# Optimization experiments

Measured on AMD Instinct MI355X. Metric: run time of the kernel, lower is better.

Reference implementation:

```python
import jax, jax.numpy as jnp
import numpy as np

E = 8       # expert_number
TOP_K = 2


def setup_inputs() -> dict:
    key = jax.random.key(0)
    ks = jax.random.split(key, 5)
    B, S, D, H = 4, 2048, 1024, 4096
    scale = 0.02
    return {
        "x": jax.random.normal(ks[0], (B, S, D), dtype=jnp.float32),
        "gate_w": jax.random.normal(ks[1], (D, E), dtype=jnp.float32) * scale,
        "gate_b": jnp.zeros((E,), dtype=jnp.float32),
        "w1": jax.random.normal(ks[2], (E, D, H), dtype=jnp.float32) * scale,
        "b1": jnp.zeros((E, H), dtype=jnp.float32),
        "w2": jax.random.normal(ks[3], (E, H, D), dtype=jnp.float32) * scale,
        "b2": jnp.zeros((E, D), dtype=jnp.float32),
    }


def reference(x, gate_w, gate_b, w1, b1, w2, b2):
    B, S, D = x.shape
    h = x.reshape(-1, D)                                   # [T, D]

    # Router: softmax in fp32, top-k, renormalize (matches torch code)
    router_logits = h @ gate_w + gate_b                    # [T, E]
    probs = jax.nn.softmax(router_logits.astype(jnp.float32), axis=-1)
    rw, sel = jax.lax.top_k(probs, TOP_K)                  # [T, K] each
    rw = rw / rw.sum(axis=-1, keepdims=True)
    rw = rw.astype(h.dtype)

    # Per-token combine weight for each expert (0 if not selected): [T, E]
    we = (jax.nn.one_hot(sel, E, dtype=h.dtype) * rw[..., None]).sum(axis=1)

    out = jnp.zeros_like(h)
    for e in range(E):  # fixed small expert count; per-expert GEMM + weighted combine
        mid = jax.nn.gelu(h @ w1[e] + b1[e], approximate=False)  # [T, H]
        ye = mid @ w2[e] + b2[e]                                 # [T, D]
        out = out + we[:, e:e + 1] * ye

    return out.reshape(B, S, D), router_logits
```

## Files before the change

kernel.cpp:

```cpp
#include <hip/hip_runtime.h>
#include <hip/hip_bf16.h>
#include <math.h>

#define T_TOKENS 8192
#define DDIM 1024
#define HDIM 4096
#define NEXP 8
#define CAP 8192
#define MAXTILES 136

typedef __bf16 bf16;
typedef __bf16 bf16x2 __attribute__((ext_vector_type(2)));
typedef __bf16 bf16x4 __attribute__((ext_vector_type(4)));
typedef __bf16 bf16x8 __attribute__((ext_vector_type(8)));
typedef float  floatx4 __attribute__((ext_vector_type(4)));

__device__ static inline void async_load16(const void* g, void* l)
{
    __builtin_amdgcn_global_load_lds(
        (const __attribute__((address_space(1))) void*)g,
        (__attribute__((address_space(3))) void*)l, 16, 0, 0);
}

__global__ void router_kernel(const float* __restrict__ x,
                              const float* __restrict__ gw,
                              const float* __restrict__ gbias,
                              float* __restrict__ logits_out,
                              int* counts, int* token_of,
                              int* selpack, int* slots, float* wts)
{
    int t = blockIdx.x;
    int l = threadIdx.x;
    const float4* xr = (const float4*)(x + (size_t)t * DDIM);

    float p[NEXP];
#pragma unroll
    for (int e = 0; e < NEXP; ++e) p[e] = 0.f;

#pragma unroll
    for (int it = 0; it < 4; ++it) {
        int d4 = it * 64 + l;
        float4 v = xr[d4];
        float vv[4] = {v.x, v.y, v.z, v.w};
#pragma unroll
        for (int j = 0; j < 4; ++j) {
            const float4* g4 = (const float4*)(gw + (size_t)(d4 * 4 + j) * NEXP);
            float4 ga = g4[0], gb4 = g4[1];
            p[0] += vv[j] * ga.x;  p[1] += vv[j] * ga.y;
            p[2] += vv[j] * ga.z;  p[3] += vv[j] * ga.w;
            p[4] += vv[j] * gb4.x; p[5] += vv[j] * gb4.y;
            p[6] += vv[j] * gb4.z; p[7] += vv[j] * gb4.w;
        }
    }
#pragma unroll
    for (int e = 0; e < NEXP; ++e) {
#pragma unroll
        for (int off = 32; off; off >>= 1) p[e] += __shfl_xor(p[e], off);
        p[e] += gbias[e];
    }
    if (l < NEXP) logits_out[(size_t)t * NEXP + l] = p[l];

    if (l == 0) {
        int e0 = 0;
#pragma unroll
        for (int e = 1; e < NEXP; ++e) if (p[e] > p[e0]) e0 = e;
        int e1 = -1;
#pragma unroll
        for (int e = 0; e < NEXP; ++e) {
            if (e == e0) continue;
            if (e1 < 0 || p[e] > p[e1]) e1 = e;
        }
        float w0 = 1.f / (1.f + expf(p[e1] - p[e0]));
        float w1 = 1.f / (1.f + expf(p[e0] - p[e1]));
        int s0 = atomicAdd(&counts[e0], 1);
        int s1 = atomicAdd(&counts[e1], 1);
        token_of[e0 * CAP + s0] = t;
        token_of[e1 * CAP + s1] = t;
        selpack[t] = e0 | (e1 << 8);
        slots[2 * t]     = s0;
        slots[2 * t + 1] = s1;
        wts[2 * t]     = w0;
        wts[2 * t + 1] = w1;
    }
}

__global__ void offsets_kernel(const int* __restrict__ counts,
                               int* __restrict__ offsets,
                               int* __restrict__ tiles,
                               int* __restrict__ ntiles)
{
    if (threadIdx.x == 0) {
        int a = 0, nt = 0;
        for (int e = 0; e < NEXP; ++e) {
            offsets[e] = a;
            for (int r = 0; r < counts[e]; r += 128)
                tiles[nt++] = (e << 24) | (a + r);
            a += counts[e];
        }
        offsets[NEXP] = a;
        *ntiles = nt;
    }
}

__global__ void gather_kernel(const float* __restrict__ x,
                              const int* __restrict__ offsets,
                              const int* __restrict__ token_of,
                              bf16* __restrict__ xg)
{
    int row = blockIdx.x * 4 + (threadIdx.x >> 6);
    int l = threadIdx.x & 63;
    int e = 0;
#pragma unroll
    for (int i = 1; i < NEXP; ++i) e += (row >= offsets[i]);
    int t = token_of[e * CAP + (row - offsets[e])];
    const float4* src = (const float4*)(x + (size_t)t * DDIM);
    bf16x4* dst = (bf16x4*)(xg + (size_t)row * DDIM);
#pragma unroll
    for (int it = 0; it < 4; ++it) {
        float4 v = src[it * 64 + l];
        bf16x4 b;
        b[0] = (bf16)v.x; b[1] = (bf16)v.y; b[2] = (bf16)v.z; b[3] = (bf16)v.w;
        dst[it * 64 + l] = b;
    }
}

__global__ void transpose_cvt_kernel(const float* __restrict__ in,
                                     bf16* __restrict__ out, int R, int C)
{
    __shared__ bf16 tile[64][68];
    int e = blockIdx.z;
    const float* src = in + (size_t)e * R * C;
    bf16* dst = out + (size_t)e * R * C;
    int r0 = blockIdx.y * 64, c0 = blockIdx.x * 64;
    int t = threadIdx.x;
    int lr = t >> 4, c4 = t & 15;
#pragma unroll
    for (int it = 0; it < 4; ++it) {
        int r = lr + it * 16;
        float4 v = *(const float4*)(src + (size_t)(r0 + r) * C + c0 + c4 * 4);
        bf16x4 b;
        b[0] = (bf16)v.x; b[1] = (bf16)v.y; b[2] = (bf16)v.z; b[3] = (bf16)v.w;
        *(bf16x4*)(&tile[r][c4 * 4]) = b;
    }
    __syncthreads();
    int oc = t >> 3, rseg = (t & 7) * 8;
#pragma unroll
    for (int it = 0; it < 2; ++it) {
        int c = oc + it * 32;
        bf16x8 v;
#pragma unroll
        for (int j = 0; j < 8; ++j) v[j] = tile[rseg + j][c];
        *(bf16x8*)(dst + (size_t)(c0 + c) * R + r0 + rseg) = v;
    }
}

template<int KTOT>
__device__ static inline void stage_tile(const bf16* __restrict__ gbase,
                                         bf16* lds, int wave, int lane, int valid)
{
#pragma unroll
    for (int it = 0; it < 4; ++it) {
        int rbase = wave * 32 + it * 8;
        int rloc  = rbase + (lane >> 3);
        int grow  = rloc < valid ? rloc : (valid - 1);
        int chunk = (lane & 7) ^ (rloc & 7);
        const bf16* g = gbase + (size_t)grow * KTOT + chunk * 8;
        async_load16(g, lds + rbase * 64);
    }
}

__device__ static inline float fast_gelu(float v)
{
    float z = v * (2.302236479f + 0.1029451170f * v * v);
    float ex = __builtin_amdgcn_exp2f(z);
    return v * ex * __builtin_amdgcn_rcpf(ex + 1.f);
}

template<int KTOT, int NTOT, bool DOGELU, typename OutT>
__global__ __launch_bounds__(256, 4)
void moe_gemm(const bf16* __restrict__ Abase, const bf16* __restrict__ Bbase,
              const float* __restrict__ bias, OutT* __restrict__ Out,
              const int* __restrict__ tiles, const int* __restrict__ ntiles,
              const int* __restrict__ offsets)
{
    if (blockIdx.x >= *ntiles) return;
    int info = tiles[blockIdx.x];
    int e = info >> 24, row0 = info & 0xffffff;
    int valid = offsets[e + 1] - row0; if (valid > 128) valid = 128;
    int n0 = blockIdx.y * 128;

    const bf16* A = Abase + (size_t)row0 * KTOT;
    const bf16* B = Bbase + (size_t)e * NTOT * KTOT + (size_t)n0 * KTOT;
    const float* bvec = bias + (size_t)e * NTOT + n0;

    __shared__ __align__(16) bf16 As[128 * 64];
    __shared__ __align__(16) bf16 Bs[128 * 64];

    int tid = threadIdx.x;
    int lane = tid & 63, wave = tid >> 6;
    int wr = wave >> 1, wc = wave & 1;
    int m16 = lane & 15, quad = lane >> 4;
    int swz = m16 & 7;

    floatx4 acc[4][4];
#pragma unroll
    for (int i = 0; i < 4; ++i)
#pragma unroll
        for (int j = 0; j < 4; ++j)
#pragma unroll
            for (int r = 0; r < 4; ++r) acc[i][j][r] = 0.f;

    for (int k0 = 0; k0 < KTOT; k0 += 64) {
        stage_tile<KTOT>(A + k0, As, wave, lane, valid);
        stage_tile<KTOT>(B + k0, Bs, wave, lane, 128);
        __syncthreads();
#pragma unroll
        for (int ks = 0; ks < 64; ks += 32) {
            int cbase = (ks >> 3) + quad;
            int pchunk = (cbase ^ swz) * 8;
            bf16x8 af[4], bfr[4];
#pragma unroll
            for (int i = 0; i < 4; ++i)
                af[i] = *(const bf16x8*)(&As[(wr * 64 + i * 16 + m16) * 64 + pchunk]);
#pragma unroll
            for (int j = 0; j < 4; ++j)
                bfr[j] = *(const bf16x8*)(&Bs[(wc * 64 + j * 16 + m16) * 64 + pchunk]);
#pragma unroll
            for (int i = 0; i < 4; ++i)
#pragma unroll
                for (int j = 0; j < 4; ++j)
                    acc[i][j] = __builtin_amdgcn_mfma_f32_16x16x32_bf16(
                        af[i], bfr[j], acc[i][j], 0, 0, 0);
        }
        __syncthreads();
    }

#pragma unroll
    for (int i = 0; i < 4; ++i) {
#pragma unroll
        for (int r = 0; r < 4; ++r) {
            int lrow = wr * 64 + i * 16 + quad * 4 + r;
            if (lrow >= valid) continue;
            size_t orow = (size_t)(row0 + lrow) * NTOT + n0;
#pragma unroll
            for (int j = 0; j < 4; ++j) {
                int lcol = wc * 64 + j * 16 + m16;
                float v = acc[i][j][r] + bvec[lcol];
                if (DOGELU) v = fast_gelu(v);
                Out[orow + lcol] = (OutT)v;
            }
        }
    }
}

__global__ void combine_kernel(const float* __restrict__ y,
                               const int* __restrict__ offsets,
                               const int* __restrict__ selpack,
                               const int* __restrict__ slots,
                               const float* __restrict__ wts,
                               float* __restrict__ out)
{
    int t = blockIdx.x;
    int sp = selpack[t];
    int e0 = sp & 0xff, e1 = (sp >> 8) & 0xff;
    int p0 = offsets[e0] + slots[2 * t];
    int p1 = offsets[e1] + slots[2 * t + 1];
    float w0 = wts[2 * t], w1 = wts[2 * t + 1];
    const float4* y0 = (const float4*)(y + (size_t)p0 * DDIM);
    const float4* y1 = (const float4*)(y + (size_t)p1 * DDIM);
    float4* o = (float4*)(out + (size_t)t * DDIM);
    int tid = threadIdx.x;
    float4 a = y0[tid], b = y1[tid];
    float4 rr;
    rr.x = w0 * a.x + w1 * b.x;
    rr.y = w0 * a.y + w1 * b.y;
    rr.z = w0 * a.z + w1 * b.z;
    rr.w = w0 * a.w + w1 * b.w;
    o[tid] = rr;
}

extern "C" void kernel_launch(void* const* d_in, const int* in_sizes, int n_in,
                              void* d_out, int out_size, void* d_ws, size_t ws_size,
                              hipStream_t stream)
{
    (void)in_sizes; (void)n_in; (void)out_size; (void)ws_size;
    const float* x  = (const float*)d_in[0];
    const float* gw = (const float*)d_in[1];
    const float* gb = (const float*)d_in[2];
    const float* w1 = (const float*)d_in[3];
    const float* b1 = (const float*)d_in[4];
    const float* w2 = (const float*)d_in[5];
    const float* b2 = (const float*)d_in[6];
    float* out    = (float*)d_out;
    float* logits = out + (size_t)T_TOKENS * DDIM;

    char* ws = (char*)d_ws;
    const size_t MB = 1024 * 1024;
    int*   counts   = (int*)(ws + 0);
    int*   offsets  = (int*)(ws + 256);
    int*   tiles    = (int*)(ws + 512);
    int*   ntiles   = (int*)(ws + 512 + 1024);
    int*   selpack  = (int*)(ws + 4096);
    int*   slots    = (int*)(ws + 4096 + 32 * 1024);
    float* wts      = (float*)(ws + 4096 + 96 * 1024);
    int*   token_of = (int*)(ws + 4096 + 160 * 1024);
    bf16*  xg  = (bf16*)(ws + 1 * MB);
    bf16*  w1b = (bf16*)(ws + 33 * MB);
    bf16*  w2b = (bf16*)(ws + 97 * MB);
    bf16*  mid = (bf16*)(ws + 161 * MB);
    float* y   = (float*)(ws + 289 * MB);

    hipMemsetAsync(counts, 0, 32, stream);

    router_kernel<<<T_TOKENS, 64, 0, stream>>>(x, gw, gb, logits, counts,
                                               token_of, selpack, slots, wts);
    offsets_kernel<<<1, 64, 0, stream>>>(counts, offsets, tiles, ntiles);
    gather_kernel<<<2 * T_TOKENS / 4, 256, 0, stream>>>(x, offsets, token_of, xg);
    transpose_cvt_kernel<<<dim3(HDIM / 64, DDIM / 64, NEXP), 256, 0, stream>>>(
        w1, w1b, DDIM, HDIM);
    transpose_cvt_kernel<<<dim3(DDIM / 64, HDIM / 64, NEXP), 256, 0, stream>>>(
        w2, w2b, HDIM, DDIM);
    moe_gemm<DDIM, HDIM, true, bf16><<<dim3(MAXTILES, HDIM / 128), 256, 0, stream>>>(
        xg, w1b, b1, mid, tiles, ntiles, offsets);
    moe_gemm<HDIM, DDIM, false, float><<<dim3(MAXTILES, DDIM / 128), 256, 0, stream>>>(
        mid, w2b, b2, y, tiles, ntiles, offsets);
    combine_kernel<<<T_TOKENS, 256, 0, stream>>>(y, offsets, selpack, slots, wts, out);
}
```

Baseline: 970.5 us.

## Fuse combine into second GEMM via atomics, switch to 32x32 MFMA, interleave tiles

The combine kernel and the fp32 intermediate y buffer are removed. The second GEMM now scales each row by its routing weight and atomically adds it into the zero-initialised output. Both GEMMs switch from 16x16x32 to 32x32x16 MFMA instructions. The tile list is interleaved across experts, with -1 padding in place of a tile count, and the router now packs 4 tokens per block. Atomic float adds make the summation order nondeterministic, and the output now needs a memset.

Result: slower. 1.049 ms (+8.1%).

```diff
diff --git a/kernel.cpp b/kernel.cpp
--- a/kernel.cpp
+++ b/kernel.cpp
@@ -10,10 +10,9 @@
 #define MAXTILES 136
 
 typedef __bf16 bf16;
-typedef __bf16 bf16x2 __attribute__((ext_vector_type(2)));
 typedef __bf16 bf16x4 __attribute__((ext_vector_type(4)));
 typedef __bf16 bf16x8 __attribute__((ext_vector_type(8)));
-typedef float  floatx4 __attribute__((ext_vector_type(4)));
+typedef float  floatx16 __attribute__((ext_vector_type(16)));
 
 __device__ static inline void async_load16(const void* g, void* l)
 {
@@ -26,11 +25,11 @@
                               const float* __restrict__ gw,
                               const float* __restrict__ gbias,
                               float* __restrict__ logits_out,
-                              int* counts, int* token_of,
-                              int* selpack, int* slots, float* wts)
-{
-    int t = blockIdx.x;
-    int l = threadIdx.x;
+                              int* counts, int* token_of, float* wtab,
+                              int* selpack)
+{
+    int t = blockIdx.x * 4 + (threadIdx.x >> 6);
+    int l = threadIdx.x & 63;
     const float4* xr = (const float4*)(x + (size_t)t * DDIM);
 
     float p[NEXP];
@@ -76,29 +75,32 @@
         int s1 = atomicAdd(&counts[e1], 1);
         token_of[e0 * CAP + s0] = t;
         token_of[e1 * CAP + s1] = t;
+        wtab[e0 * CAP + s0] = w0;
+        wtab[e1 * CAP + s1] = w1;
         selpack[t] = e0 | (e1 << 8);
-        slots[2 * t]     = s0;
-        slots[2 * t + 1] = s1;
-        wts[2 * t]     = w0;
-        wts[2 * t + 1] = w1;
     }
 }
 
 __global__ void offsets_kernel(const int* __restrict__ counts,
                                int* __restrict__ offsets,
-                               int* __restrict__ tiles,
-                               int* __restrict__ ntiles)
+                               int* __restrict__ tiles)
 {
     if (threadIdx.x == 0) {
+        int tmp[MAXTILES];
         int a = 0, nt = 0;
         for (int e = 0; e < NEXP; ++e) {
             offsets[e] = a;
             for (int r = 0; r < counts[e]; r += 128)
-                tiles[nt++] = (e << 24) | (a + r);
+                tmp[nt++] = (e << 24) | (a + r);
             a += counts[e];
         }
         offsets[NEXP] = a;
-        *ntiles = nt;
+        int per = (nt + 7) >> 3;
+        for (int p = 0; p < MAXTILES; ++p) {
+            int c = p & 7, k = p >> 3;
+            int src = c * per + k;
+            tiles[p] = (k < per && src < nt) ? tmp[src] : -1;
+        }
     }
 }
 
@@ -176,107 +178,118 @@
     return v * ex * __builtin_amdgcn_rcpf(ex + 1.f);
 }
 
-template<int KTOT, int NTOT, bool DOGELU, typename OutT>
+#define GEMM_CORE(KTOT)                                                        \
+    int tid = threadIdx.x;                                                     \
+    int lane = tid & 63, wave = tid >> 6;                                      \
+    int wr = wave >> 1, wc = wave & 1;                                         \
+    int m32 = lane & 31, khalf = lane >> 5;                                    \
+    int swz = m32 & 7;                                                         \
+    floatx16 acc[2][2];                                                        \
+    _Pragma("unroll") for (int i = 0; i < 2; ++i)                              \
+    _Pragma("unroll") for (int j = 0; j < 2; ++j)                              \
+    _Pragma("unroll") for (int r = 0; r < 16; ++r) acc[i][j][r] = 0.f;         \
+    for (int k0 = 0; k0 < KTOT; k0 += 64) {                                    \
+        stage_tile<KTOT>(A + k0, As, wave, lane, valid);                       \
+        stage_tile<KTOT>(B + k0, Bs, wave, lane, 128);                         \
+        __syncthreads();                                                       \
+        _Pragma("unroll") for (int s = 0; s < 4; ++s) {                        \
+            int pofs = (((2 * s + khalf) ^ swz) * 8);                          \
+            bf16x8 af[2], bfr[2];                                              \
+            _Pragma("unroll") for (int i = 0; i < 2; ++i)                      \
+                af[i] = *(const bf16x8*)(&As[(wr * 64 + i * 32 + m32) * 64 + pofs]); \
+            _Pragma("unroll") for (int j = 0; j < 2; ++j)                      \
+                bfr[j] = *(const bf16x8*)(&Bs[(wc * 64 + j * 32 + m32) * 64 + pofs]); \
+            _Pragma("unroll") for (int i = 0; i < 2; ++i)                      \
+            _Pragma("unroll") for (int j = 0; j < 2; ++j)                      \
+                acc[i][j] = __builtin_amdgcn_mfma_f32_32x32x16_bf16(           \
+                    af[i], bfr[j], acc[i][j], 0, 0, 0);                        \
+        }                                                                      \
+        __syncthreads();                                                       \
+    }
+
 __global__ __launch_bounds__(256, 4)
-void moe_gemm(const bf16* __restrict__ Abase, const bf16* __restrict__ Bbase,
-              const float* __restrict__ bias, OutT* __restrict__ Out,
-              const int* __restrict__ tiles, const int* __restrict__ ntiles,
-              const int* __restrict__ offsets)
-{
-    if (blockIdx.x >= *ntiles) return;
+void moe_gemm1(const bf16* __restrict__ Abase, const bf16* __restrict__ Bbase,
+               const float* __restrict__ bias, bf16* __restrict__ Out,
+               const int* __restrict__ tiles, const int* __restrict__ offsets)
+{
     int info = tiles[blockIdx.x];
+    if (info < 0) return;
     int e = info >> 24, row0 = info & 0xffffff;
     int valid = offsets[e + 1] - row0; if (valid > 128) valid = 128;
     int n0 = blockIdx.y * 128;
 
-    const bf16* A = Abase + (size_t)row0 * KTOT;
-    const bf16* B = Bbase + (size_t)e * NTOT * KTOT + (size_t)n0 * KTOT;
-    const float* bvec = bias + (size_t)e * NTOT + n0;
+    const bf16* A = Abase + (size_t)row0 * DDIM;
+    const bf16* B = Bbase + (size_t)e * HDIM * DDIM + (size_t)n0 * DDIM;
+    const float* bvec = bias + (size_t)e * HDIM + n0;
 
     __shared__ __align__(16) bf16 As[128 * 64];
     __shared__ __align__(16) bf16 Bs[128 * 64];
 
-    int tid = threadIdx.x;
-    int lane = tid & 63, wave = tid >> 6;
-    int wr = wave >> 1, wc = wave & 1;
-    int m16 = lane & 15, quad = lane >> 4;
-    int swz = m16 & 7;
-
-    floatx4 acc[4][4];
-#pragma unroll
-    for (int i = 0; i < 4; ++i)
-#pragma unroll
-        for (int j = 0; j < 4; ++j)
-#pragma unroll
-            for (int r = 0; r < 4; ++r) acc[i][j][r] = 0.f;
-
-    for (int k0 = 0; k0 < KTOT; k0 += 64) {
-        stage_tile<KTOT>(A + k0, As, wave, lane, valid);
-        stage_tile<KTOT>(B + k0, Bs, wave, lane, 128);
-        __syncthreads();
-#pragma unroll
-        for (int ks = 0; ks < 64; ks += 32) {
-            int cbase = (ks >> 3) + quad;
-            int pchunk = (cbase ^ swz) * 8;
-            bf16x8 af[4], bfr[4];
-#pragma unroll
-            for (int i = 0; i < 4; ++i)
-                af[i] = *(const bf16x8*)(&As[(wr * 64 + i * 16 + m16) * 64 + pchunk]);
-#pragma unroll
-            for (int j = 0; j < 4; ++j)
-                bfr[j] = *(const bf16x8*)(&Bs[(wc * 64 + j * 16 + m16) * 64 + pchunk]);
-#pragma unroll
-            for (int i = 0; i < 4; ++i)
-#pragma unroll
-                for (int j = 0; j < 4; ++j)
-                    acc[i][j] = __builtin_amdgcn_mfma_f32_16x16x32_bf16(
-                        af[i], bfr[j], acc[i][j], 0, 0, 0);
-        }
-        __syncthreads();
-    }
-
-#pragma unroll
-    for (int i = 0; i < 4; ++i) {
-#pragma unroll
-        for (int r = 0; r < 4; ++r) {
-            int lrow = wr * 64 + i * 16 + quad * 4 + r;
-            if (lrow >= valid) continue;
-            size_t orow = (size_t)(row0 + lrow) * NTOT + n0;
-#pragma unroll
-            for (int j = 0; j < 4; ++j) {
-                int lcol = wc * 64 + j * 16 + m16;
-                float v = acc[i][j][r] + bvec[lcol];
-                if (DOGELU) v = fast_gelu(v);
-                Out[orow + lcol] = (OutT)v;
+    GEMM_CORE(DDIM)
+
+#pragma unroll
+    for (int i = 0; i < 2; ++i) {
+#pragma unroll
+        for (int j = 0; j < 2; ++j) {
+            int lcol = wc * 64 + j * 32 + m32;
+            float bj = bvec[lcol];
+#pragma unroll
+            for (int r = 0; r < 16; ++r) {
+                int lrow = wr * 64 + i * 32 + (r & 3) + 8 * (r >> 2) + 4 * khalf;
+                if (lrow >= valid) continue;
+                float v = acc[i][j][r] + bj;
+                Out[(size_t)(row0 + lrow) * HDIM + n0 + lcol] = (bf16)fast_gelu(v);
             }
         }
     }
 }
 
-__global__ void combine_kernel(const float* __restrict__ y,
-                               const int* __restrict__ offsets,
-                               const int* __restrict__ selpack,
-                               const int* __restrict__ slots,
-                               const float* __restrict__ wts,
-                               float* __restrict__ out)
-{
-    int t = blockIdx.x;
-    int sp = selpack[t];
-    int e0 = sp & 0xff, e1 = (sp >> 8) & 0xff;
-    int p0 = offsets[e0] + slots[2 * t];
-    int p1 = offsets[e1] + slots[2 * t + 1];
-    float w0 = wts[2 * t], w1 = wts[2 * t + 1];
-    const float4* y0 = (const float4*)(y + (size_t)p0 * DDIM);
-    const float4* y1 = (const float4*)(y + (size_t)p1 * DDIM);
-    float4* o = (float4*)(out + (size_t)t * DDIM);
-    int tid = threadIdx.x;
-    float4 a = y0[tid], b = y1[tid];
-    float4 rr;
-    rr.x = w0 * a.x + w1 * b.x;
-    rr.y = w0 * a.y + w1 * b.y;
-    rr.z = w0 * a.z + w1 * b.z;
-    rr.w = w0 * a.w + w1 * b.w;
-    o[tid] = rr;
+__global__ __launch_bounds__(256, 4)
+void moe_gemm2(const bf16* __restrict__ Abase, const bf16* __restrict__ Bbase,
+               const float* __restrict__ bias, float* __restrict__ out,
+               const int* __restrict__ tiles, const int* __restrict__ offsets,
+               const int* __restrict__ token_of, const float* __restrict__ wtab)
+{
+    int info = tiles[blockIdx.x];
+    if (info < 0) return;
+    int e = info >> 24, row0 = info & 0xffffff;
+    int valid = offsets[e + 1] - row0; if (valid > 128) valid = 128;
+    int n0 = blockIdx.y * 128;
+
+    const bf16* A = Abase + (size_t)row0 * HDIM;
+    const bf16* B = Bbase + (size_t)e * DDIM * HDIM + (size_t)n0 * HDIM;
+    const float* bvec = bias + (size_t)e * DDIM + n0;
+
+    __shared__ __align__(16) bf16 As[128 * 64];
+    __shared__ __align__(16) bf16 Bs[128 * 64];
+
+    GEMM_CORE(HDIM)
+
+    int*   tokS = (int*)As;
+    float* wgtS = (float*)As + 128;
+    if (tid < valid) {
+        int s = row0 + tid - offsets[e];
+        tokS[tid] = token_of[e * CAP + s];
+        wgtS[tid] = wtab[e * CAP + s];
+    }
+    __syncthreads();
+
+#pragma unroll
+    for (int i = 0; i < 2; ++i) {
+#pragma unroll
+        for (int j = 0; j < 2; ++j) {
+            int lcol = wc * 64 + j * 32 + m32;
+            float bj = bvec[lcol];
+#pragma unroll
+            for (int r = 0; r < 16; ++r) {
+                int lrow = wr * 64 + i * 32 + (r & 3) + 8 * (r >> 2) + 4 * khalf;
+                if (lrow >= valid) continue;
+                float v = acc[i][j][r] + bj;
+                unsafeAtomicAdd(out + (size_t)tokS[lrow] * DDIM + n0 + lcol,
+                                wgtS[lrow] * v);
+            }
+        }
+    }
 }
 
 extern "C" void kernel_launch(void* const* d_in, const int* in_sizes, int n_in,
@@ -299,30 +312,27 @@
     int*   counts   = (int*)(ws + 0);
     int*   offsets  = (int*)(ws + 256);
     int*   tiles    = (int*)(ws + 512);
-    int*   ntiles   = (int*)(ws + 512 + 1024);
     int*   selpack  = (int*)(ws + 4096);
-    int*   slots    = (int*)(ws + 4096 + 32 * 1024);
-    float* wts      = (float*)(ws + 4096 + 96 * 1024);
-    int*   token_of = (int*)(ws + 4096 + 160 * 1024);
+    int*   token_of = (int*)(ws + 4096 + 64 * 1024);
+    float* wtab     = (float*)(ws + 4096 + 320 * 1024);
     bf16*  xg  = (bf16*)(ws + 1 * MB);
     bf16*  w1b = (bf16*)(ws + 33 * MB);
     bf16*  w2b = (bf16*)(ws + 97 * MB);
     bf16*  mid = (bf16*)(ws + 161 * MB);
-    float* y   = (float*)(ws + 289 * MB);
 
     hipMemsetAsync(counts, 0, 32, stream);
-
-    router_kernel<<<T_TOKENS, 64, 0, stream>>>(x, gw, gb, logits, counts,
-                                               token_of, selpack, slots, wts);
-    offsets_kernel<<<1, 64, 0, stream>>>(counts, offsets, tiles, ntiles);
+    hipMemsetAsync(out, 0, (size_t)T_TOKENS * DDIM * sizeof(float), stream);
+
+    router_kernel<<<T_TOKENS / 4, 256, 0, stream>>>(x, gw, gb, logits, counts,
+                                                    token_of, wtab, selpack);
+    offsets_kernel<<<1, 64, 0, stream>>>(counts, offsets, tiles);
     gather_kernel<<<2 * T_TOKENS / 4, 256, 0, stream>>>(x, offsets, token_of, xg);
     transpose_cvt_kernel<<<dim3(HDIM / 64, DDIM / 64, NEXP), 256, 0, stream>>>(
         w1, w1b, DDIM, HDIM);
     transpose_cvt_kernel<<<dim3(DDIM / 64, HDIM / 64, NEXP), 256, 0, stream>>>(
         w2, w2b, HDIM, DDIM);
-    moe_gemm<DDIM, HDIM, true, bf16><<<dim3(MAXTILES, HDIM / 128), 256, 0, stream>>>(
-        xg, w1b, b1, mid, tiles, ntiles, offsets);
-    moe_gemm<HDIM, DDIM, false, float><<<dim3(MAXTILES, DDIM / 128), 256, 0, stream>>>(
-        mid, w2b, b2, y, tiles, ntiles, offsets);
-    combine_kernel<<<T_TOKENS, 256, 0, stream>>>(y, offsets, selpack, slots, wts, out);
-}
+    moe_gemm1<<<dim3(MAXTILES, HDIM / 128), 256, 0, stream>>>(
+        xg, w1b, b1, mid, tiles, offsets);
+    moe_gemm2<<<dim3(MAXTILES, DDIM / 128), 256, 0, stream>>>(
+        mid, w2b, b2, out, tiles, offsets, token_of, wtab);
+}
```
